# Kernel tuning notes

Measured on AMD Instinct MI355X. Metric: run time of the kernel, lower is better.

Reference implementation:

```python
import jax, jax.numpy as jnp
import numpy as np

N_NODES = 50000
N_EDGES = 400000
D = 128


def _rgg_layer(x, src, tgt, Wk, Wq, Wv, Ws, b, n_nodes):
    # Node-level projections (dense GEMMs, as in PyG which applies Linear before message passing)
    k = x @ Wk  # lin_key, gathered at targets
    q = x @ Wq  # lin_query, gathered at sources
    v = x @ Wv  # lin_value, gathered at sources
    # Per-edge gather + sigmoid gate + elementwise message
    eta = jax.nn.sigmoid(k[tgt] + q[src])  # [E, D]
    msg = eta * v[src]                      # [E, D]
    # Scatter-add aggregation to target nodes
    agg = jax.ops.segment_sum(msg, tgt, num_segments=n_nodes)
    # Root/skip connection + bias
    return agg + x @ Ws + b


def setup_inputs() -> dict:
    key = jax.random.key(0)
    ks = jax.random.split(key, 12)
    s = 1.0 / np.sqrt(D)
    x = jax.random.normal(ks[0], (N_NODES, D), dtype=jnp.float32)
    edge_index = jax.random.randint(ks[1], (2, N_EDGES), 0, N_NODES, dtype=jnp.int64)
    W = lambda k: (jax.random.normal(k, (D, D), dtype=jnp.float32) * s)
    return {
        "x": x,
        "edge_index": edge_index,
        "Wk1": W(ks[2]), "Wq1": W(ks[3]), "Wv1": W(ks[4]), "Ws1": W(ks[5]),
        "b1": jnp.zeros((D,), dtype=jnp.float32),
        "Wk2": W(ks[6]), "Wq2": W(ks[7]), "Wv2": W(ks[8]), "Ws2": W(ks[9]),
        "b2": jnp.zeros((D,), dtype=jnp.float32),
    }


def reference(x, edge_index, Wk1, Wq1, Wv1, Ws1, b1, Wk2, Wq2, Wv2, Ws2, b2):
    src, tgt = edge_index[0], edge_index[1]
    n = x.shape[0]
    h = _rgg_layer(x, src, tgt, Wk1, Wq1, Wv1, Ws1, b1, n)
    h = jax.nn.relu(h)
    # F.dropout treated as identity (deterministic/inference reference)
    out = _rgg_layer(h, src, tgt, Wk2, Wq2, Wv2, Ws2, b2, n)
    return out
```

## Files before the change

### kernel.cpp

```cpp
#include <hip/hip_runtime.h>

#define N_NODES 50000
#define D 128
#define N_EDGES 400000
#define NCHUNKS ((N_NODES + 255) / 256)
#define NBLK64 ((N_NODES + 63) / 64)
#define W_FRAG_SHORTS 16384

#define CVT_BLOCKS 3125
#define MW_BLOCKS  64
#define HIST_BLOCKS ((N_EDGES + 255) / 256)
#define PREP_BLOCKS (CVT_BLOCKS + MW_BLOCKS + HIST_BLOCKS)

typedef short s8v  __attribute__((ext_vector_type(8)));
typedef float f4v  __attribute__((ext_vector_type(4)));

__device__ __forceinline__ unsigned int f2bf(float f) {
    unsigned int u = __float_as_uint(f);
    u += 0x7FFFu + ((u >> 16) & 1u);
    return u >> 16;
}
__device__ __forceinline__ unsigned int packbf(float a, float b) {
    return (f2bf(b) << 16) | f2bf(a);
}
__device__ __forceinline__ float bflo(unsigned int u) { return __uint_as_float(u << 16); }
__device__ __forceinline__ float bfhi(unsigned int u) { return __uint_as_float(u & 0xFFFF0000u); }
__device__ __forceinline__ float sigm(float x) {
    return __builtin_amdgcn_rcpf(1.f + __expf(-x));
}

__global__ __launch_bounds__(256)
void prep_all(const float* __restrict__ X, short* __restrict__ Xb,
              const float* __restrict__ W0, const float* __restrict__ W1,
              const float* __restrict__ W2, const float* __restrict__ W3,
              const float* __restrict__ W4, const float* __restrict__ W5,
              const float* __restrict__ W6, const float* __restrict__ W7,
              short* __restrict__ Wt,
              const int* __restrict__ tgt, int* __restrict__ counts)
{
    const int b = blockIdx.x;
    if (b < CVT_BLOCKS) {
        const size_t i = ((size_t)b * 256 + threadIdx.x) * 8;
        float4 a0 = *(const float4*)(X + i);
        float4 a1 = *(const float4*)(X + i + 4);
        s8v v;
        v[0] = (short)f2bf(a0.x); v[1] = (short)f2bf(a0.y);
        v[2] = (short)f2bf(a0.z); v[3] = (short)f2bf(a0.w);
        v[4] = (short)f2bf(a1.x); v[5] = (short)f2bf(a1.y);
        v[6] = (short)f2bf(a1.z); v[7] = (short)f2bf(a1.w);
        *(s8v*)(Xb + i) = v;
    } else if (b < CVT_BLOCKS + MW_BLOCKS) {
        const int bb   = b - CVT_BLOCKS;
        const int wsel = bb >> 3;
        const float* W = (wsel == 0) ? W0 : (wsel == 1) ? W1 : (wsel == 2) ? W2 :
                         (wsel == 3) ? W3 : (wsel == 4) ? W4 : (wsel == 5) ? W5 :
                         (wsel == 6) ? W6 : W7;
        const int slot = (bb & 7) * 256 + threadIdx.x;
        const int frag = slot >> 6;
        const int lane = slot & 63;
        const int n    = (frag >> 2) * 16 + (lane & 15);
        const int kc   = frag & 3;
        const int quad = lane >> 4;
        const int k0   = kc * 32 + quad * 8;
        s8v v;
#pragma unroll
        for (int j = 0; j < 8; ++j)
            v[j] = (short)f2bf(W[(size_t)(k0 + j) * D + n]);
        *(s8v*)(Wt + (size_t)wsel * W_FRAG_SHORTS + (size_t)slot * 8) = v;
    } else {
        const int e = (b - CVT_BLOCKS - MW_BLOCKS) * 256 + threadIdx.x;
        if (e < N_EDGES) atomicAdd(&counts[tgt[e]], 1);
    }
}

__global__ __launch_bounds__(256)
void gemm_all(const short* __restrict__ Xb, const short* __restrict__ WtL,
              const float* __restrict__ bias,
              short* __restrict__ Kb, unsigned int* __restrict__ QV,
              float* __restrict__ Agg)
{
    __shared__ __align__(16) short As[8192];
    __shared__ __align__(16) short Bs[16384];
    __shared__ __align__(16) float biasS[128];

    const int tid  = threadIdx.x;
    const int lane = tid & 63;
    const int w    = tid >> 6;
    const int wr   = w & 1;
    const int wc   = w >> 1;
    const int m0   = blockIdx.x * 64;

    if (tid < 128) biasS[tid] = bias[tid];

#pragma unroll
    for (int i = 0; i < 4; ++i) {
        const int m   = (tid >> 4) + 16 * i;
        const int oct = tid & 15;
        const int row = m0 + m;
        s8v v = (s8v){0, 0, 0, 0, 0, 0, 0, 0};
        if (row < N_NODES) v = *(const s8v*)(Xb + (size_t)row * D + oct * 8);
        const int kc = oct >> 2, quad = oct & 3;
        const int frag = (m >> 4) * 4 + kc;
        const int slot = ((m & 15) + 16 * quad) ^ (kc << 1);
        *(s8v*)&As[frag * 512 + slot * 8] = v;
    }

    float* Cs = (float*)Bs;

    for (int sel = 0; sel < 4; ++sel) {
        __syncthreads();

        const short* Wf = WtL + (size_t)sel * W_FRAG_SHORTS;
#pragma unroll
        for (int j = 0; j < 8; ++j) {
            const int chunk = tid + 256 * j;
            __builtin_amdgcn_global_load_lds(
                (const __attribute__((address_space(1))) unsigned int*)(Wf + chunk * 8),
                (__attribute__((address_space(3))) unsigned int*)(&Bs[(chunk & ~63) * 8]),
                16, 0, 0);
        }
        __syncthreads();

        f4v acc[2][4];
#pragma unroll
        for (int mt = 0; mt < 2; ++mt)
#pragma unroll
            for (int nt = 0; nt < 4; ++nt)
                acc[mt][nt] = (f4v){0.f, 0.f, 0.f, 0.f};

#pragma unroll
        for (int kc = 0; kc < 4; ++kc) {
            const int sl = (lane ^ (kc << 1)) * 8;
            s8v a0 = *(const s8v*)&As[((2 * wr + 0) * 4 + kc) * 512 + sl];
            s8v a1 = *(const s8v*)&As[((2 * wr + 1) * 4 + kc) * 512 + sl];
#pragma unroll
            for (int nt = 0; nt < 4; ++nt) {
                s8v b = *(const s8v*)&Bs[((4 * wc + nt) * 4 + kc) * 512 + lane * 8];
                acc[0][nt] = __builtin_amdgcn_mfma_f32_16x16x32_bf16(a0, b, acc[0][nt], 0, 0, 0);
                acc[1][nt] = __builtin_amdgcn_mfma_f32_16x16x32_bf16(a1, b, acc[1][nt], 0, 0, 0);
            }
        }
        __syncthreads();

#pragma unroll
        for (int mt = 0; mt < 2; ++mt) {
            const int r0 = wr * 32 + mt * 16 + (lane >> 4) * 4;
#pragma unroll
            for (int nt = 0; nt < 4; ++nt) {
                const int col = wc * 64 + nt * 16 + (lane & 15);
                const int g = col >> 2, jj = col & 3;
#pragma unroll
                for (int i = 0; i < 4; ++i) {
                    const int row = r0 + i;
                    const int gs  = g ^ (((row >> 2) & 3) << 2);
                    Cs[row * 128 + gs * 4 + jj] = acc[mt][nt][i];
                }
            }
        }
        __syncthreads();

#pragma unroll
        for (int j = 0; j < 8; ++j) {
            const int c    = tid + 256 * j;
            const int row  = c >> 5;
            const int gg   = c & 31;
            const int gs   = gg ^ (((row >> 2) & 3) << 2);
            const f4v vv   = *(const f4v*)&Cs[row * 128 + gs * 4];
            const int grow = m0 + row;
            if (grow >= N_NODES) continue;
            if (sel == 3) {
                const float4 bv = *(const float4*)&biasS[gg * 4];
                float4 o = make_float4(vv[0] + bv.x, vv[1] + bv.y,
                                       vv[2] + bv.z, vv[3] + bv.w);
                *(float4*)&Agg[(size_t)grow * D + gg * 4] = o;
            } else {
                const unsigned int p0 = packbf(vv[0], vv[1]);
                const unsigned int p1 = packbf(vv[2], vv[3]);
                if (sel == 0) {
                    uint2* kp = (uint2*)((unsigned int*)Kb + (size_t)grow * 64 + gg * 2);
                    *kp = make_uint2(p0, p1);
                } else {
                    unsigned int* rowp = QV + (size_t)grow * 128 + gg * 4 + (sel == 2 ? 1 : 0);
                    rowp[0] = p0; rowp[2] = p1;
                }
            }
        }
    }
}

__global__ __launch_bounds__(256)
void chunk_reduce(const int* __restrict__ counts, int* __restrict__ chunk_sum)
{
    __shared__ int s[256];
    int i = blockIdx.x * 256 + threadIdx.x;
    s[threadIdx.x] = (i < N_NODES) ? counts[i] : 0;
    __syncthreads();
    for (int d = 128; d > 0; d >>= 1) {
        if (threadIdx.x < d) s[threadIdx.x] += s[threadIdx.x + d];
        __syncthreads();
    }
    if (threadIdx.x == 0) chunk_sum[blockIdx.x] = s[0];
}

__global__ __launch_bounds__(256)
void scan_sums(const int* __restrict__ chunk_sum,
               int* __restrict__ chunk_off, int* __restrict__ off)
{
    __shared__ int s[256];
    const int tid = threadIdx.x;
    const int v = (tid < NCHUNKS) ? chunk_sum[tid] : 0;
    s[tid] = v;
    __syncthreads();
    for (int d = 1; d < 256; d <<= 1) {
        int t = (tid >= d) ? s[tid - d] : 0;
        __syncthreads();
        s[tid] += t;
        __syncthreads();
    }
    if (tid < NCHUNKS) chunk_off[tid] = s[tid] - v;
    if (tid == NCHUNKS - 1) off[N_NODES] = s[tid];
}

__global__ __launch_bounds__(256)
void scan_chunks(const int* __restrict__ counts, const int* __restrict__ chunk_off,
                 int* __restrict__ off, int* __restrict__ cursor)
{
    __shared__ int s[256];
    int i = blockIdx.x * 256 + threadIdx.x;
    int v = (i < N_NODES) ? counts[i] : 0;
    s[threadIdx.x] = v;
    __syncthreads();
    for (int d = 1; d < 256; d <<= 1) {
        int t = (threadIdx.x >= d) ? s[threadIdx.x - d] : 0;
        __syncthreads();
        s[threadIdx.x] += t;
        __syncthreads();
    }
    if (i < N_NODES) {
        int excl = s[threadIdx.x] - v + chunk_off[blockIdx.x];
        off[i]    = excl;
        cursor[i] = excl;
    }
}

__global__ __launch_bounds__(256)
void scatter_kernel(const int* __restrict__ src, const int* __restrict__ tgt,
                    int* __restrict__ cursor, int* __restrict__ es)
{
    int e = blockIdx.x * 256 + threadIdx.x;
    if (e < N_EDGES) {
        int pos = atomicAdd(&cursor[tgt[e]], 1);
        es[pos] = src[e];
    }
}

template<bool FIRST>
__global__ __launch_bounds__(256)
void node_agg(const int* __restrict__ off, const int* __restrict__ es,
              const short* __restrict__ K, const unsigned int* __restrict__ QV,
              const float* __restrict__ Skip, float* __restrict__ OutF,
              unsigned int* __restrict__ Hb)
{
    const int lane = threadIdx.x & 63;
    const int t    = __builtin_amdgcn_readfirstlane(blockIdx.x * 4 + (threadIdx.x >> 6));

    const unsigned int ku = ((const unsigned int*)K)[(size_t)t * 64 + lane];
    const float kx = bflo(ku), ky = bfhi(ku);
    const float2 sk = ((const float2*)Skip)[(size_t)t * 64 + lane];

    float ax = 0.f, ay = 0.f, bx = 0.f, by = 0.f;
    float cx = 0.f, cy = 0.f, dx = 0.f, dy = 0.f;
    const int e0 = __builtin_amdgcn_readfirstlane(off[t]);
    const int e1 = __builtin_amdgcn_readfirstlane(off[t + 1]);

    int e = e0;
    for (; e + 4 <= e1; e += 4) {
        const int s0 = __builtin_amdgcn_readfirstlane(es[e]);
        const int s1 = __builtin_amdgcn_readfirstlane(es[e + 1]);
        const int s2 = __builtin_amdgcn_readfirstlane(es[e + 2]);
        const int s3 = __builtin_amdgcn_readfirstlane(es[e + 3]);
        const uint2 qv0 = ((const uint2*)(QV + (size_t)s0 * 128))[lane];
        const uint2 qv1 = ((const uint2*)(QV + (size_t)s1 * 128))[lane];
        const uint2 qv2 = ((const uint2*)(QV + (size_t)s2 * 128))[lane];
        const uint2 qv3 = ((const uint2*)(QV + (size_t)s3 * 128))[lane];
        ax += bflo(qv0.y) * sigm(kx + bflo(qv0.x));
        ay += bfhi(qv0.y) * sigm(ky + bfhi(qv0.x));
        bx += bflo(qv1.y) * sigm(kx + bflo(qv1.x));
        by += bfhi(qv1.y) * sigm(ky + bfhi(qv1.x));
        cx += bflo(qv2.y) * sigm(kx + bflo(qv2.x));
        cy += bfhi(qv2.y) * sigm(ky + bfhi(qv2.x));
        dx += bflo(qv3.y) * sigm(kx + bflo(qv3.x));
        dy += bfhi(qv3.y) * sigm(ky + bfhi(qv3.x));
    }
    for (; e < e1; ++e) {
        const int s0 = __builtin_amdgcn_readfirstlane(es[e]);
        const uint2 qv0 = ((const uint2*)(QV + (size_t)s0 * 128))[lane];
        ax += bflo(qv0.y) * sigm(kx + bflo(qv0.x));
        ay += bfhi(qv0.y) * sigm(ky + bfhi(qv0.x));
    }

    const float rx = sk.x + (ax + bx) + (cx + dx);
    const float ry = sk.y + (ay + by) + (cy + dy);

    if (FIRST) {
        Hb[(size_t)t * 64 + lane] = packbf(fmaxf(rx, 0.f), fmaxf(ry, 0.f));
    } else {
        ((float2*)OutF)[(size_t)t * 64 + lane] = make_float2(rx, ry);
    }
}

extern "C" void kernel_launch(void* const* d_in, const int* in_sizes, int n_in,
                              void* d_out, int out_size, void* d_ws, size_t ws_size,
                              hipStream_t stream)
{
    const float* x   = (const float*)d_in[0];
    const int*   ei  = (const int*)d_in[1];
    const float* Wk1 = (const float*)d_in[2];
    const float* Wq1 = (const float*)d_in[3];
    const float* Wv1 = (const float*)d_in[4];
    const float* Ws1 = (const float*)d_in[5];
    const float* b1  = (const float*)d_in[6];
    const float* Wk2 = (const float*)d_in[7];
    const float* Wq2 = (const float*)d_in[8];
    const float* Wv2 = (const float*)d_in[9];
    const float* Ws2 = (const float*)d_in[10];
    const float* b2  = (const float*)d_in[11];

    const int* src = ei;
    const int* tgt = ei + N_EDGES;

    const size_t nd = (size_t)N_NODES * D;
    short* kb  = (short*)d_ws;
    short* qv  = kb + nd;
    short* xb  = qv + 2 * nd;
    short* hb  = xb + nd;
    float* agg1 = (float*)(hb + nd);
    short* wt  = (short*)(agg1 + nd);
    int* counts    = (int*)(wt + 8 * W_FRAG_SHORTS);
    int* off       = counts + N_NODES;
    int* cursor    = off + N_NODES + 1;
    int* es        = cursor + N_NODES;
    int* chunk_sum = es + N_EDGES;
    int* chunk_off = chunk_sum + NCHUNKS;
    float* out = (float*)d_out;

    hipMemsetAsync(counts, 0, N_NODES * sizeof(int), stream);
    prep_all<<<PREP_BLOCKS, 256, 0, stream>>>(x, xb,
                                              Wk1, Wq1, Wv1, Ws1, Wk2, Wq2, Wv2, Ws2,
                                              wt, tgt, counts);
    chunk_reduce  <<<NCHUNKS, 256, 0, stream>>>(counts, chunk_sum);
    scan_sums     <<<1, 256, 0, stream>>>(chunk_sum, chunk_off, off);
    scan_chunks   <<<NCHUNKS, 256, 0, stream>>>(counts, chunk_off, off, cursor);
    scatter_kernel<<<HIST_BLOCKS, 256, 0, stream>>>(src, tgt, cursor, es);

    gemm_all<<<NBLK64, 256, 0, stream>>>(xb, wt, b1, kb, (unsigned int*)qv, agg1);
    node_agg<true><<<N_NODES / 4, 256, 0, stream>>>(off, es, kb, (const unsigned int*)qv,
                                                    agg1, nullptr, (unsigned int*)hb);

    gemm_all<<<NBLK64, 256, 0, stream>>>(hb, wt + 4 * W_FRAG_SHORTS, b2,
                                         kb, (unsigned int*)qv, out);
    node_agg<false><<<N_NODES / 4, 256, 0, stream>>>(off, es, kb, (const unsigned int*)qv,
                                                     out, out, nullptr);
}
```

Measured before the change: 268.7 us.

## Fuse CSR scan into one grid-synced kernel and overlap scatter with GEMM1

Replaces the three-kernel prefix scan (chunk reduce, single-block scan, chunk scan) with one kernel in which each block publishes its chunk sum and spin-waits on a global counter, then sums the earlier chunk totals itself. The edge scatter kernel is merged into the first GEMM launch as extra blocks, so the scatter's atomic traffic can run alongside the MFMA tiles. This cuts four launches and their gaps down to two. The spin wait assumes all 196 scan blocks are resident at once, which risks deadlock if that ever fails, and off[N_NODES] is now hardcoded to the edge count.

```diff
diff --git a/kernel.cpp b/kernel.cpp
--- a/kernel.cpp
+++ b/kernel.cpp
@@ -74,21 +74,64 @@
 }
 
 __global__ __launch_bounds__(256)
-void gemm_all(const short* __restrict__ Xb, const short* __restrict__ WtL,
-              const float* __restrict__ bias,
-              short* __restrict__ Kb, unsigned int* __restrict__ QV,
-              float* __restrict__ Agg)
-{
-    __shared__ __align__(16) short As[8192];
-    __shared__ __align__(16) short Bs[16384];
-    __shared__ __align__(16) float biasS[128];
-
+void csr_scan(const int* __restrict__ counts, int* __restrict__ off,
+              int* __restrict__ cursor, int* __restrict__ done_ctr,
+              int* __restrict__ chunk_sum)
+{
+    __shared__ int s[256];
+    const int b = blockIdx.x, t = threadIdx.x;
+    const int i = b * 256 + t;
+    const int v = (i < N_NODES) ? counts[i] : 0;
+    s[t] = v;
+    __syncthreads();
+    for (int d = 1; d < 256; d <<= 1) {
+        int tt = (t >= d) ? s[t - d] : 0;
+        __syncthreads();
+        s[t] += tt;
+        __syncthreads();
+    }
+    const int incl = s[t];
+
+    if (t == 255) {
+        __hip_atomic_store(&chunk_sum[b], incl, __ATOMIC_RELAXED, __HIP_MEMORY_SCOPE_AGENT);
+        __hip_atomic_fetch_add(done_ctr, 1, __ATOMIC_RELEASE, __HIP_MEMORY_SCOPE_AGENT);
+    }
+    if (t == 0) {
+        while (__hip_atomic_load(done_ctr, __ATOMIC_ACQUIRE, __HIP_MEMORY_SCOPE_AGENT) < NCHUNKS)
+            __builtin_amdgcn_s_sleep(8);
+    }
+    __syncthreads();
+
+    const int pv = (t < b) ? __hip_atomic_load(&chunk_sum[t], __ATOMIC_RELAXED,
+                                               __HIP_MEMORY_SCOPE_AGENT) : 0;
+    __syncthreads();
+    s[t] = pv;
+    __syncthreads();
+    for (int d = 128; d > 0; d >>= 1) {
+        if (t < d) s[t] += s[t + d];
+        __syncthreads();
+    }
+    const int base = s[0];
+
+    if (i < N_NODES) {
+        const int excl = base + incl - v;
+        off[i]    = excl;
+        cursor[i] = excl;
+    }
+    if (b == 0 && t == 0) off[N_NODES] = N_EDGES;
+}
+
+__device__ __forceinline__
+void gemm_tile(int m0, const short* __restrict__ Xb, const short* __restrict__ WtL,
+               const float* __restrict__ bias, short* __restrict__ Kb,
+               unsigned int* __restrict__ QV, float* __restrict__ Agg,
+               short* As, short* Bs, float* biasS)
+{
     const int tid  = threadIdx.x;
     const int lane = tid & 63;
     const int w    = tid >> 6;
     const int wr   = w & 1;
     const int wc   = w >> 1;
-    const int m0   = blockIdx.x * 64;
 
     if (tid < 128) biasS[tid] = bias[tid];
 
@@ -189,69 +232,38 @@
 }
 
 __global__ __launch_bounds__(256)
-void chunk_reduce(const int* __restrict__ counts, int* __restrict__ chunk_sum)
-{
-    __shared__ int s[256];
-    int i = blockIdx.x * 256 + threadIdx.x;
-    s[threadIdx.x] = (i < N_NODES) ? counts[i] : 0;
-    __syncthreads();
-    for (int d = 128; d > 0; d >>= 1) {
-        if (threadIdx.x < d) s[threadIdx.x] += s[threadIdx.x + d];
-        __syncthreads();
-    }
-    if (threadIdx.x == 0) chunk_sum[blockIdx.x] = s[0];
-}
-
-__global__ __launch_bounds__(256)
-void scan_sums(const int* __restrict__ chunk_sum,
-               int* __restrict__ chunk_off, int* __restrict__ off)
-{
-    __shared__ int s[256];
-    const int tid = threadIdx.x;
-    const int v = (tid < NCHUNKS) ? chunk_sum[tid] : 0;
-    s[tid] = v;
-    __syncthreads();
-    for (int d = 1; d < 256; d <<= 1) {
-        int t = (tid >= d) ? s[tid - d] : 0;
-        __syncthreads();
-        s[tid] += t;
-        __syncthreads();
-    }
-    if (tid < NCHUNKS) chunk_off[tid] = s[tid] - v;
-    if (tid == NCHUNKS - 1) off[N_NODES] = s[tid];
-}
-
-__global__ __launch_bounds__(256)
-void scan_chunks(const int* __restrict__ counts, const int* __restrict__ chunk_off,
-                 int* __restrict__ off, int* __restrict__ cursor)
-{
-    __shared__ int s[256];
-    int i = blockIdx.x * 256 + threadIdx.x;
-    int v = (i < N_NODES) ? counts[i] : 0;
-    s[threadIdx.x] = v;
-    __syncthreads();
-    for (int d = 1; d < 256; d <<= 1) {
-        int t = (threadIdx.x >= d) ? s[threadIdx.x - d] : 0;
-        __syncthreads();
-        s[threadIdx.x] += t;
-        __syncthreads();
-    }
-    if (i < N_NODES) {
-        int excl = s[threadIdx.x] - v + chunk_off[blockIdx.x];
-        off[i]    = excl;
-        cursor[i] = excl;
-    }
-}
-
-__global__ __launch_bounds__(256)
-void scatter_kernel(const int* __restrict__ src, const int* __restrict__ tgt,
-                    int* __restrict__ cursor, int* __restrict__ es)
-{
-    int e = blockIdx.x * 256 + threadIdx.x;
-    if (e < N_EDGES) {
-        int pos = atomicAdd(&cursor[tgt[e]], 1);
-        es[pos] = src[e];
-    }
+void gemm1_scatter(const short* __restrict__ Xb, const short* __restrict__ WtL,
+                   const float* __restrict__ bias,
+                   short* __restrict__ Kb, unsigned int* __restrict__ QV,
+                   float* __restrict__ Agg,
+                   const int* __restrict__ src, const int* __restrict__ tgt,
+                   int* __restrict__ cursor, int* __restrict__ es)
+{
+    __shared__ __align__(16) short As[8192];
+    __shared__ __align__(16) short Bs[16384];
+    __shared__ __align__(16) float biasS[128];
+
+    if (blockIdx.x < NBLK64) {
+        gemm_tile(blockIdx.x * 64, Xb, WtL, bias, Kb, QV, Agg, As, Bs, biasS);
+    } else {
+        const int e = (blockIdx.x - NBLK64) * 256 + threadIdx.x;
+        if (e < N_EDGES) {
+            int pos = atomicAdd(&cursor[tgt[e]], 1);
+            es[pos] = src[e];
+        }
+    }
+}
+
+__global__ __launch_bounds__(256)
+void gemm_all(const short* __restrict__ Xb, const short* __restrict__ WtL,
+              const float* __restrict__ bias,
+              short* __restrict__ Kb, unsigned int* __restrict__ QV,
+              float* __restrict__ Agg)
+{
+    __shared__ __align__(16) short As[8192];
+    __shared__ __align__(16) short Bs[16384];
+    __shared__ __align__(16) float biasS[128];
+    gemm_tile(blockIdx.x * 64, Xb, WtL, bias, Kb, QV, Agg, As, Bs, biasS);
 }
 
 template<bool FIRST>
@@ -330,30 +342,28 @@
     const int* tgt = ei + N_EDGES;
 
     const size_t nd = (size_t)N_NODES * D;
-    short* kb  = (short*)d_ws;
-    short* qv  = kb + nd;
-    short* xb  = qv + 2 * nd;
-    short* hb  = xb + nd;
+    short* kb   = (short*)d_ws;
+    short* qv   = kb + nd;
+    short* xb   = qv + 2 * nd;
+    short* hb   = xb + nd;
     float* agg1 = (float*)(hb + nd);
-    short* wt  = (short*)(agg1 + nd);
+    short* wt   = (short*)(agg1 + nd);
     int* counts    = (int*)(wt + 8 * W_FRAG_SHORTS);
-    int* off       = counts + N_NODES;
+    int* done_ctr  = counts + N_NODES;
+    int* off       = counts + N_NODES + 2;
     int* cursor    = off + N_NODES + 1;
     int* es        = cursor + N_NODES;
     int* chunk_sum = es + N_EDGES;
-    int* chunk_off = chunk_sum + NCHUNKS;
     float* out = (float*)d_out;
 
-    hipMemsetAsync(counts, 0, N_NODES * sizeof(int), stream);
+    hipMemsetAsync(counts, 0, (N_NODES + 2) * sizeof(int), stream);
     prep_all<<<PREP_BLOCKS, 256, 0, stream>>>(x, xb,
                                               Wk1, Wq1, Wv1, Ws1, Wk2, Wq2, Wv2, Ws2,
                                               wt, tgt, counts);
-    chunk_reduce  <<<NCHUNKS, 256, 0, stream>>>(counts, chunk_sum);
-    scan_sums     <<<1, 256, 0, stream>>>(chunk_sum, chunk_off, off);
-    scan_chunks   <<<NCHUNKS, 256, 0, stream>>>(counts, chunk_off, off, cursor);
-    scatter_kernel<<<HIST_BLOCKS, 256, 0, stream>>>(src, tgt, cursor, es);
-
-    gemm_all<<<NBLK64, 256, 0, stream>>>(xb, wt, b1, kb, (unsigned int*)qv, agg1);
+    csr_scan<<<NCHUNKS, 256, 0, stream>>>(counts, off, cursor, done_ctr, chunk_sum);
+
+    gemm1_scatter<<<NBLK64 + HIST_BLOCKS, 256, 0, stream>>>(
+        xb, wt, b1, kb, (unsigned int*)qv, agg1, src, tgt, cursor, es);
     node_agg<true><<<N_NODES / 4, 256, 0, stream>>>(off, es, kb, (const unsigned int*)qv,
                                                     agg1, nullptr, (unsigned int*)hb);
 
```

New measurement: 269.2 us. About the same (+0.2%).
